# Kernel optimization log

Hardware: AMD Instinct MI355X
Metric: run time of the kernel (lower is better)

## Reference

```python
import jax, jax.numpy as jnp
import numpy as np

N_QUBITS = 6
N_QLAYERS = 3
LOGISTIC_R = 3.99
HENON_A, HENON_B = 1.4, 0.3


def _conv1d(x, w, b):
    # x: [B, C_in, T], w: [C_out, C_in, K=3], SAME padding (pad=1)
    y = jax.lax.conv_general_dilated(x, w, window_strides=(1,), padding=((1, 1),),
                                     dimension_numbers=('NCH', 'OIH', 'NCH'))
    return y + b[None, :, None]


def _apply_1q_batched(state, G, q):
    # state: [B,2,...,2], G: [B,2,2] acting on qubit axis 1+q
    s = jnp.moveaxis(state, 1 + q, -1)
    s = jnp.einsum('bij,b...j->b...i', G, s)
    return jnp.moveaxis(s, -1, 1 + q)


def _apply_1q(state, G, q):
    s = jnp.moveaxis(state, 1 + q, -1)
    s = jnp.einsum('ij,b...j->b...i', G, s)
    return jnp.moveaxis(s, -1, 1 + q)


def _apply_cnot(state, c, t):
    s = jnp.moveaxis(state, (1 + c, 1 + t), (-2, -1))
    # control=1 block: flip target amplitudes
    s = jnp.concatenate([s[..., 0:1, :], s[..., 1:2, ::-1]], axis=-2)
    return jnp.moveaxis(s, (-2, -1), (1 + c, 1 + t))


def quantum_expvals(angles, qweights):
    # angles: [B, 6] real encoding angles; qweights: [3, 6] shared RY params
    B = angles.shape[0]
    state = jnp.zeros((B, 2 ** N_QUBITS), jnp.complex64).at[:, 0].set(1.0)
    state = state.reshape((B,) + (2,) * N_QUBITS)
    half = 0.5 * angles
    for i in range(N_QUBITS):
        ax = half[:, i % N_QUBITS]
        ay = half[:, (i + 1) % N_QUBITS]
        az = half[:, (i + 2) % N_QUBITS]
        cx_, sx_ = jnp.cos(ax), jnp.sin(ax)
        RX = jnp.stack([jnp.stack([cx_ + 0j, -1j * sx_], -1),
                        jnp.stack([-1j * sx_, cx_ + 0j], -1)], -2)
        state = _apply_1q_batched(state, RX, i)
        cy_, sy_ = jnp.cos(ay), jnp.sin(ay)
        RY = jnp.stack([jnp.stack([cy_ + 0j, -sy_ + 0j], -1),
                        jnp.stack([sy_ + 0j, cy_ + 0j], -1)], -2)
        state = _apply_1q_batched(state, RY, i)
        ez = jnp.exp(1j * az)
        zero = jnp.zeros_like(ez)
        RZ = jnp.stack([jnp.stack([jnp.conj(ez), zero], -1),
                        jnp.stack([zero, ez], -1)], -2)
        state = _apply_1q_batched(state, RZ, i)
    for l in range(N_QLAYERS):
        for q in range(N_QUBITS):
            a = 0.5 * qweights[l, q]
            c_, s_ = jnp.cos(a), jnp.sin(a)
            RY = jnp.array([[1., 0.], [0., 1.]], jnp.float32) * c_ + \
                 jnp.array([[0., -1.], [1., 0.]], jnp.float32) * s_
            state = _apply_1q(state, RY.astype(jnp.complex64), q)
        for q in range(N_QUBITS):
            state = _apply_cnot(state, q, (q + 1) % N_QUBITS)
    probs = (state * jnp.conj(state)).real  # [B,2,...,2]
    evs = []
    for i in range(N_QUBITS):
        axes = tuple(a for a in range(1, N_QUBITS + 1) if a != 1 + i)
        p = jnp.sum(probs, axis=axes)  # [B,2]
        evs.append(p[:, 0] - p[:, 1])
    return jnp.stack(evs, -1)  # [B,6]


def _lstm_cell(xt, h, c, Wih, Whh, bih, bhh):
    g = xt @ Wih.T + bih + h @ Whh.T + bhh
    i, f, gg, o = jnp.split(g, 4, axis=-1)
    c2 = jax.nn.sigmoid(f) * c + jax.nn.sigmoid(i) * jnp.tanh(gg)
    h2 = jax.nn.sigmoid(o) * jnp.tanh(c2)
    return h2, c2


def _forward(x, w0, b0, w1, b1, w2, b2, Wih, Whh, bih, bhh, qweights, Wfc, bfc, Wout, bout):
    B = x.shape[0]
    t = x.transpose(0, 2, 1)                 # [B, C, T]
    t = jax.nn.relu(_conv1d(t, w0, b0))
    t = jax.nn.relu(_conv1d(t, w1, b1))
    t = jax.nn.relu(_conv1d(t, w2, b2))
    t = t.transpose(2, 0, 1)                 # [T, B, H]
    H = t.shape[2]
    h0 = jnp.zeros((B, H), x.dtype)
    c0 = jnp.zeros((B, H), x.dtype)

    def step(carry, xt):
        h, c = carry
        h, c = _lstm_cell(xt, h, c, Wih, Whh, bih, bhh)
        h = LOGISTIC_R * h * (1.0 - h)
        x0, y0 = h[:, 0], h[:, 1]
        xn = 1.0 - HENON_A * x0 ** 2 + y0
        yn = HENON_B * x0
        h = jnp.concatenate([xn[:, None], yn[:, None], h[:, 2:]], axis=1)
        # QuantumRNNCell called as qrnn(hx, hx): h = h + fc(quantum(h[:, :6]))
        h = h + quantum_expvals(h[:, :N_QUBITS], qweights) @ Wfc.T + bfc
        return (h, c), None

    (h, _), _ = jax.lax.scan(step, (h0, c0), t)
    return jax.nn.sigmoid(h @ Wout.T + bout)  # [B, 1]


def setup_inputs() -> dict:
    key = jax.random.key(0)
    ks = jax.random.split(key, 20)
    B, T, D, Htcn, Hlstm = 1024, 256, 64, 32, 32
    s = 0.1
    inp = {
        'x': jax.random.normal(ks[0], (B, T, D), jnp.float32),
        'w0': jax.random.normal(ks[1], (Htcn, D, 3), jnp.float32) * s,
        'b0': jax.random.normal(ks[2], (Htcn,), jnp.float32) * s,
        'w1': jax.random.normal(ks[3], (Htcn, Htcn, 3), jnp.float32) * s,
        'b1': jax.random.normal(ks[4], (Htcn,), jnp.float32) * s,
        'w2': jax.random.normal(ks[5], (Htcn, Htcn, 3), jnp.float32) * s,
        'b2': jax.random.normal(ks[6], (Htcn,), jnp.float32) * s,
        'Wih': jax.random.normal(ks[7], (4 * Hlstm, Htcn), jnp.float32) * s,
        'Whh': jax.random.normal(ks[8], (4 * Hlstm, Hlstm), jnp.float32) * s,
        'bih': jax.random.normal(ks[9], (4 * Hlstm,), jnp.float32) * s,
        'bhh': jax.random.normal(ks[10], (4 * Hlstm,), jnp.float32) * s,
        'qweights': jax.random.normal(ks[11], (N_QLAYERS, N_QUBITS), jnp.float32),
        'Wfc': jax.random.normal(ks[12], (Hlstm, N_QUBITS), jnp.float32) * s,
        'bfc': jax.random.normal(ks[13], (Hlstm,), jnp.float32) * s,
        'Wout': jax.random.normal(ks[14], (1, Hlstm), jnp.float32) * s,
        'bout': jax.random.normal(ks[15], (1,), jnp.float32) * s,
    }
    return inp


def reference(x, w0, b0, w1, b1, w2, b2, Wih, Whh, bih, bhh, qweights, Wfc, bfc, Wout, bout):
    return _forward(x, w0, b0, w1, b1, w2, b2, Wih, Whh, bih, bhh, qweights, Wfc, bfc, Wout, bout)
```

## Files before the change

kernel.cpp:

```cpp
#include <hip/hip_runtime.h>

#define B_SIZE 1024
#define T_LEN  256
#define D_IN   64
#define HC     32

typedef int v2i_t __attribute__((ext_vector_type(2)));

__device__ __forceinline__ float frcp(float x){ return __builtin_amdgcn_rcpf(x); }
__device__ __forceinline__ float rfl(float x){
    return __uint_as_float(__builtin_amdgcn_readfirstlane(__float_as_uint(x)));
}
__device__ __forceinline__ float rdlane(float x, int l){
    return __int_as_float(__builtin_amdgcn_readlane(__float_as_int(x), l));
}
__device__ __forceinline__ float ftanh(float x){
    return 1.f - 2.f*frcp(__expf(2.f*x) + 1.f);
}
__device__ __forceinline__ float fsigmoid(float x){
    return frcp(1.f + __expf(-x));
}

template<int CTRL>
__device__ __forceinline__ int dppmov(int x){
    return __builtin_amdgcn_update_dpp(x, x, CTRL, 0xF, 0xF, false);
}

template<int M>
__device__ __forceinline__ int dpp_xor(int x){
    static_assert(M >= 1 && M <= 15, "dpp_xor mask");
    constexpr int hi = M & 12;
    constexpr int q  = (hi == 4 || hi == 12) ? ((M & 3) ^ 3) : (M & 3);
    if constexpr (q == 1) x = dppmov<0xB1>(x);
    else if constexpr (q == 2) x = dppmov<0x4E>(x);
    else if constexpr (q == 3) x = dppmov<0x1B>(x);
    if constexpr (hi == 4)       x = dppmov<0x141>(x);
    else if constexpr (hi == 8)  x = dppmov<0x128>(x);
    else if constexpr (hi == 12) x = dppmov<0x140>(x);
    return x;
}

template<int M>
__device__ __forceinline__ float xshuf(float xf, unsigned lane){
    (void)lane;
    if constexpr (M == 0) return xf;
    int x = __float_as_int(xf);
    if constexpr (M & 16){
        x = __builtin_amdgcn_ds_swizzle(x, ((M & 31) << 10) | 0x1F);
    } else if constexpr (M & 15){
        x = dpp_xor<M & 15>(x);
    }
    if constexpr (M & 32){
        v2i_t r = __builtin_amdgcn_permlane32_swap(x, x, false, false);
        x = r.x ^ r.y ^ x;
    }
    return __int_as_float(x);
}

struct QMasks { int M[3][6]; int S[3][6]; int R[6]; };
constexpr QMasks qmasks(){
    QMasks qm{};
    unsigned m[6], n[6];
    for (int i = 0; i < 6; i++){ m[i] = 1u << i; n[i] = 1u << i; }
    for (int l = 0; l < 3; l++){
        for (int q = 0; q < 6; q++){
            unsigned u = m[q], r = 0;
            for (int i = 0; i < 6; i++) if ((u >> i) & 1u) r |= (32u >> i);
            qm.S[l][q] = (int)r;
            unsigned u2 = 0;
            for (int i = 0; i < 6; i++) u2 |= ((n[i] >> q) & 1u) << i;
            unsigned r2 = 0;
            for (int i = 0; i < 6; i++) if ((u2 >> i) & 1u) r2 |= (32u >> i);
            qm.M[l][q] = (int)r2;
        }
        for (int q = 0; q < 6; q++) m[(q + 1) % 6] ^= m[q];
        n[0] ^= n[5];
        for (int q = 4; q >= 0; q--) n[q + 1] ^= n[q];
    }
    for (int i = 0; i < 6; i++){
        unsigned u = m[i], r = 0;
        for (int j = 0; j < 6; j++) if ((u >> j) & 1u) r |= (32u >> j);
        qm.R[i] = (int)r;
    }
    return qm;
}
constexpr QMasks QM = qmasks();

__global__ __launch_bounds__(256) void conv0_kernel(const float* __restrict__ x,
    const float* __restrict__ w0, const float* __restrict__ b0, float* __restrict__ out)
{
    __shared__ float xs[130*65];
    __shared__ float wl[192*32];
    const int tid = threadIdx.x;
    const int b  = blockIdx.x >> 1;
    const int s0 = (blockIdx.x & 1) * 128;

    for (int idx = tid; idx < 130*64; idx += 256){
        int r = idx >> 6, d = idx & 63;
        int s = s0 - 1 + r;
        float v = 0.f;
        if (s >= 0 && s < T_LEN) v = x[(size_t)b*(T_LEN*D_IN) + (size_t)s*D_IN + d];
        xs[r*65 + d] = v;
    }
    for (int idx = tid; idx < 192*32; idx += 256){
        int r = idx >> 5, c = idx & 31;
        wl[idx] = w0[c*192 + r];
    }
    __syncthreads();

    const int c0 = (tid & 7) * 4;
    const int sl = (tid >> 3) * 4;
    float acc[4][4];
    #pragma unroll
    for (int ci = 0; ci < 4; ci++){
        float bb = b0[c0+ci];
        #pragma unroll
        for (int m = 0; m < 4; m++) acc[ci][m] = bb;
    }
    for (int d = 0; d < 64; d++){
        float xv[6];
        #pragma unroll
        for (int o = 0; o < 6; o++) xv[o] = xs[(sl+o)*65 + d];
        #pragma unroll
        for (int kk = 0; kk < 3; kk++){
            const float4 wv = *(const float4*)&wl[(d*3+kk)*32 + c0];
            float w4[4] = {wv.x, wv.y, wv.z, wv.w};
            #pragma unroll
            for (int ci = 0; ci < 4; ci++)
                #pragma unroll
                for (int m = 0; m < 4; m++)
                    acc[ci][m] += xv[m+kk]*w4[ci];
        }
    }
    #pragma unroll
    for (int ci = 0; ci < 4; ci++){
        float4 v;
        v.x = fmaxf(acc[ci][0], 0.f); v.y = fmaxf(acc[ci][1], 0.f);
        v.z = fmaxf(acc[ci][2], 0.f); v.w = fmaxf(acc[ci][3], 0.f);
        *(float4*)&out[(size_t)b*(HC*T_LEN) + (size_t)(c0+ci)*T_LEN + (s0+sl)] = v;
    }
}

template<bool TOUT>
__global__ __launch_bounds__(256) void convm_kernel(const float* __restrict__ in,
    const float* __restrict__ w, const float* __restrict__ bias, float* __restrict__ out)
{
    __shared__ float xs[130*33];
    __shared__ float wl[96*32];
    const int tid = threadIdx.x;
    const int b  = blockIdx.x >> 1;
    const int s0 = (blockIdx.x & 1) * 128;

    for (int idx = tid; idx < 32*130; idx += 256){
        int ci = idx / 130; int r = idx - ci*130;
        int s = s0 - 1 + r;
        float v = 0.f;
        if (s >= 0 && s < T_LEN) v = in[(size_t)b*(HC*T_LEN) + (size_t)ci*T_LEN + s];
        xs[r*33 + ci] = v;
    }
    for (int idx = tid; idx < 96*32; idx += 256){
        int r = idx >> 5, c = idx & 31;
        wl[idx] = w[c*96 + r];
    }
    __syncthreads();

    const int c0 = (tid & 7) * 4;
    const int sl = (tid >> 3) * 4;
    float acc[4][4];
    #pragma unroll
    for (int ci = 0; ci < 4; ci++){
        float bb = bias[c0+ci];
        #pragma unroll
        for (int m = 0; m < 4; m++) acc[ci][m] = bb;
    }
    for (int ci2 = 0; ci2 < 32; ci2++){
        float xv[6];
        #pragma unroll
        for (int o = 0; o < 6; o++) xv[o] = xs[(sl+o)*33 + ci2];
        #pragma unroll
        for (int kk = 0; kk < 3; kk++){
            const float4 wv = *(const float4*)&wl[(ci2*3+kk)*32 + c0];
            float w4[4] = {wv.x, wv.y, wv.z, wv.w};
            #pragma unroll
            for (int ci = 0; ci < 4; ci++)
                #pragma unroll
                for (int m = 0; m < 4; m++)
                    acc[ci][m] += xv[m+kk]*w4[ci];
        }
    }
    if (!TOUT){
        #pragma unroll
        for (int ci = 0; ci < 4; ci++){
            float4 v;
            v.x = fmaxf(acc[ci][0], 0.f); v.y = fmaxf(acc[ci][1], 0.f);
            v.z = fmaxf(acc[ci][2], 0.f); v.w = fmaxf(acc[ci][3], 0.f);
            *(float4*)&out[(size_t)b*(HC*T_LEN) + (size_t)(c0+ci)*T_LEN + (s0+sl)] = v;
        }
    } else {
        #pragma unroll
        for (int m = 0; m < 4; m++){
            int s = s0 + sl + m;
            float4 v;
            v.x = fmaxf(acc[0][m], 0.f); v.y = fmaxf(acc[1][m], 0.f);
            v.z = fmaxf(acc[2][m], 0.f); v.w = fmaxf(acc[3][m], 0.f);
            *(float4*)&out[(size_t)s*(B_SIZE*HC) + (size_t)b*HC + c0] = v;
        }
    }
}

__global__ __launch_bounds__(256, 1) void scan_kernel(
    const float* __restrict__ tS,
    const float* __restrict__ Wih, const float* __restrict__ Whh,
    const float* __restrict__ bih, const float* __restrict__ bhh,
    const float* __restrict__ qw,  const float* __restrict__ Wfc,
    const float* __restrict__ bfc, const float* __restrict__ Wout,
    const float* __restrict__ bout, float* __restrict__ out)
{
    const unsigned lane = threadIdx.x & 63u;
    const int wv   = threadIdx.x >> 6;
    const int b    = __builtin_amdgcn_readfirstlane(blockIdx.x * 4 + wv);
    const int r1 = lane, r2 = lane + 64;
    const int k  = lane & 31;

    float wA[32], wB[32], uA[32], uB[32];
    #pragma unroll
    for (int j4 = 0; j4 < 8; j4++){
        float4 a  = ((const float4*)Wih)[r1*8 + j4];
        float4 c_ = ((const float4*)Wih)[r2*8 + j4];
        float4 d_ = ((const float4*)Whh)[r1*8 + j4];
        float4 e  = ((const float4*)Whh)[r2*8 + j4];
        wA[j4*4+0]=a.x;  wA[j4*4+1]=a.y;  wA[j4*4+2]=a.z;  wA[j4*4+3]=a.w;
        wB[j4*4+0]=c_.x; wB[j4*4+1]=c_.y; wB[j4*4+2]=c_.z; wB[j4*4+3]=c_.w;
        uA[j4*4+0]=d_.x; uA[j4*4+1]=d_.y; uA[j4*4+2]=d_.z; uA[j4*4+3]=d_.w;
        uB[j4*4+0]=e.x;  uB[j4*4+1]=e.y;  uB[j4*4+2]=e.z;  uB[j4*4+3]=e.w;
    }
    const float bias1 = bih[r1] + bhh[r1];
    const float bias2 = bih[r2] + bhh[r2];

    float wfcr[6];
    #pragma unroll
    for (int j = 0; j < 6; j++) wfcr[j] = Wfc[k*6 + j];
    const float bfcl  = bfc[k];
    const float woutl = (lane < 32) ? Wout[k] : 0.f;
    const float boutv = bout[0];

    float cgv[18], ssin[18];
    #pragma unroll
    for (int g = 0; g < 18; g++){
        int l = g / 6, q = g % 6;
        float a = 0.5f * qw[g];
        float cv = __cosf(a), sv = __sinf(a);
        cgv[g] = rfl(cv);
        unsigned sm = (unsigned)QM.S[l][q];
        ssin[g] = (__builtin_popcount(sm & lane) & 1) ? sv : -sv;
    }
    float wsgn[6];
    #pragma unroll
    for (int j = 0; j < 6; j++) wsgn[j] = (lane & (1u << j)) ? -1.f : 1.f;
    const bool qs[6] = { (lane & 32u) != 0, (lane & 16u) != 0, (lane & 8u) != 0,
                         (lane & 4u) != 0,  (lane & 2u) != 0,  (lane & 1u) != 0 };

    float h = 0.f, c = 0.f;
    const float* xbase = tS + (size_t)b * HC;

    float4 xf[8];
    #pragma unroll
    for (int j4 = 0; j4 < 8; j4++) xf[j4] = ((const float4*)xbase)[j4];

    #pragma clang loop unroll(disable)
    for (int s = 0; s < T_LEN; s++){
        float xt[32];
        #pragma unroll
        for (int j4 = 0; j4 < 8; j4++){
            xt[j4*4+0]=xf[j4].x; xt[j4*4+1]=xf[j4].y; xt[j4*4+2]=xf[j4].z; xt[j4*4+3]=xf[j4].w;
        }
        {
            int s2 = (s + 1 < T_LEN) ? s + 1 : s;
            const float4* np_ = (const float4*)(xbase + (size_t)s2*(B_SIZE*HC));
            #pragma unroll
            for (int j4 = 0; j4 < 8; j4++) xf[j4] = np_[j4];
        }

        float a1a = bias1, a1b = 0.f, a2a = bias2, a2b = 0.f;
        #pragma unroll
        for (int j = 0; j < 32; j += 2){
            a1a += xt[j]*wA[j];     a1b += xt[j+1]*wA[j+1];
            a2a += xt[j]*wB[j];     a2b += xt[j+1]*wB[j+1];
        }
        #pragma unroll
        for (int j = 0; j < 32; j += 2){
            float h0 = rdlane(h, j), h1 = rdlane(h, j+1);
            a1a += h0*uA[j];   a1b += h1*uA[j+1];
            a2a += h0*uB[j];   a2b += h1*uB[j+1];
        }
        float acc1 = a1a + a1b, acc2 = a2a + a2b;

        float sigA = fsigmoid(acc1);
        float argB = (lane < 32) ? acc2 : 0.5f*acc2;
        float tt   = ftanh(argB);
        float actB = (lane < 32) ? tt : (0.5f + 0.5f*tt);
        float fsig = xshuf<32>(sigA, lane);
        float osig = xshuf<32>(actB, lane);
        c = fsig*c + sigA*actB;
        float hn = osig * ftanh(c);

        hn = 3.99f * hn * (1.f - hn);
        float x0 = rdlane(hn, 0), y0 = rdlane(hn, 1);
        float xnv = 1.f - 1.4f*x0*x0 + y0;
        float ynv = 0.3f * x0;

        float ang[6];
        ang[0] = 0.5f*xnv; ang[1] = 0.5f*ynv;
        ang[2] = 0.5f*rdlane(hn, 2); ang[3] = 0.5f*rdlane(hn, 3);
        ang[4] = 0.5f*rdlane(hn, 4); ang[5] = 0.5f*rdlane(hn, 5);
        float ca[6], sa[6];
        #pragma unroll
        for (int j = 0; j < 6; j++){ ca[j] = __cosf(ang[j]); sa[j] = __sinf(ang[j]); }

        float fr[6], fi[6];
        #pragma unroll
        for (int i = 0; i < 6; i++){
            const int i1 = (i+1)%6, i2 = (i+2)%6;
            float cx=ca[i], sx=sa[i], cy=ca[i1], sy=sa[i1], cz=ca[i2], sz=sa[i2];
            float w0r = cy*cx, w0i = sy*sx;
            float w1r = sy*cx, w1i = -cy*sx;
            float q0r = cz*w0r + sz*w0i, q0i = cz*w0i - sz*w0r;
            float q1r = cz*w1r - sz*w1i, q1i = cz*w1i + sz*w1r;
            fr[i] = qs[i] ? q1r : q0r;
            fi[i] = qs[i] ? q1i : q0i;
        }
        float t01r = fr[0]*fr[1] - fi[0]*fi[1], t01i = fr[0]*fi[1] + fi[0]*fr[1];
        float t23r = fr[2]*fr[3] - fi[2]*fi[3], t23i = fr[2]*fi[3] + fi[2]*fr[3];
        float t45r = fr[4]*fr[5] - fi[4]*fi[5], t45i = fr[4]*fi[5] + fi[4]*fr[5];
        float t03r = t01r*t23r - t01i*t23i,     t03i = t01r*t23i + t01i*t23r;
        float ar   = t03r*t45r - t03i*t45i,     ai   = t03r*t45i + t03i*t45r;

        #define GATE(L,Q) { \
            constexpr int MM = QM.M[L][Q]; \
            float br = xshuf<MM>(ar, lane), bi = xshuf<MM>(ai, lane); \
            float cg = cgv[(L)*6+(Q)], ss = ssin[(L)*6+(Q)]; \
            ar = cg*ar + ss*br; ai = cg*ai + ss*bi; }
        GATE(0,0) GATE(0,1) GATE(0,2) GATE(0,3) GATE(0,4) GATE(0,5)
        GATE(1,0) GATE(1,1) GATE(1,2) GATE(1,3) GATE(1,4) GATE(1,5)
        GATE(2,0) GATE(2,1) GATE(2,2) GATE(2,3) GATE(2,4) GATE(2,5)
        #undef GATE

        float wp = ar*ar + ai*ai;
        wp = wsgn[0]*wp + xshuf< 1>(wp, lane);
        wp = wsgn[1]*wp + xshuf< 2>(wp, lane);
        wp = wsgn[2]*wp + xshuf< 4>(wp, lane);
        wp = wsgn[3]*wp + xshuf< 8>(wp, lane);
        wp = wsgn[4]*wp + xshuf<16>(wp, lane);
        wp = wsgn[5]*wp + xshuf<32>(wp, lane);
        float ev0 = rdlane(wp, QM.R[0]), ev1 = rdlane(wp, QM.R[1]);
        float ev2 = rdlane(wp, QM.R[2]), ev3 = rdlane(wp, QM.R[3]);
        float ev4 = rdlane(wp, QM.R[4]), ev5 = rdlane(wp, QM.R[5]);

        float upd = bfcl + (wfcr[0]*ev0 + wfcr[1]*ev1)
                         + (wfcr[2]*ev2 + wfcr[3]*ev3)
                         + (wfcr[4]*ev4 + wfcr[5]*ev5);

        float hsel = hn;
        hsel = (lane == 0u) ? xnv : hsel;
        hsel = (lane == 1u) ? ynv : hsel;
        h = hsel + upd;
    }

    float pv = (lane < 32) ? h*woutl : 0.f;
    #pragma unroll
    for (int off = 32; off; off >>= 1) pv += __shfl_xor(pv, off, 64);
    if (lane == 0) out[b] = fsigmoid(pv + boutv);
}

extern "C" void kernel_launch(void* const* d_in, const int* in_sizes, int n_in,
                              void* d_out, int out_size, void* d_ws, size_t ws_size,
                              hipStream_t stream)
{
    (void)in_sizes; (void)n_in; (void)out_size; (void)ws_size;
    const float* x    = (const float*)d_in[0];
    const float* w0   = (const float*)d_in[1];
    const float* b0   = (const float*)d_in[2];
    const float* w1   = (const float*)d_in[3];
    const float* b1   = (const float*)d_in[4];
    const float* w2   = (const float*)d_in[5];
    const float* b2   = (const float*)d_in[6];
    const float* Wih  = (const float*)d_in[7];
    const float* Whh  = (const float*)d_in[8];
    const float* bih  = (const float*)d_in[9];
    const float* bhh  = (const float*)d_in[10];
    const float* qw   = (const float*)d_in[11];
    const float* Wfc  = (const float*)d_in[12];
    const float* bfc  = (const float*)d_in[13];
    const float* Wout = (const float*)d_in[14];
    const float* bout = (const float*)d_in[15];
    float* out = (float*)d_out;

    float* t0 = (float*)d_ws;
    float* t1 = t0 + (size_t)B_SIZE*HC*T_LEN;
    float* tS = t0;

    conv0_kernel<<<2048, 256, 0, stream>>>(x, w0, b0, t0);
    convm_kernel<false><<<2048, 256, 0, stream>>>(t0, w1, b1, t1);
    convm_kernel<true ><<<2048, 256, 0, stream>>>(t1, w2, b2, tS);
    scan_kernel<<<256, 256, 0, stream>>>(tS, Wih, Whh, bih, bhh, qw, Wfc, bfc, Wout, bout, out);
}
```

Before: 681.0 us.

## Hoist LSTM input projection out of recurrent scan into parallel gates kernel

```diff
diff --git a/kernel.cpp b/kernel.cpp
--- a/kernel.cpp
+++ b/kernel.cpp
@@ -5,7 +5,8 @@
 #define D_IN   64
 #define HC     32
 
-typedef int v2i_t __attribute__((ext_vector_type(2)));
+typedef int   v2i_t __attribute__((ext_vector_type(2)));
+typedef float v2f   __attribute__((ext_vector_type(2)));
 
 __device__ __forceinline__ float frcp(float x){ return __builtin_amdgcn_rcpf(x); }
 __device__ __forceinline__ float rfl(float x){
@@ -40,15 +41,24 @@
     return x;
 }
 
+#if defined(__has_builtin)
+#  if __has_builtin(__builtin_amdgcn_permlane16_swap)
+#    define HAVE_PL16 1
+#  endif
+#endif
+
 template<int M>
-__device__ __forceinline__ float xshuf(float xf, unsigned lane){
-    (void)lane;
+__device__ __forceinline__ float xshuf(float xf){
     if constexpr (M == 0) return xf;
     int x = __float_as_int(xf);
+    if constexpr (M & 15) x = dpp_xor<M & 15>(x);
     if constexpr (M & 16){
-        x = __builtin_amdgcn_ds_swizzle(x, ((M & 31) << 10) | 0x1F);
-    } else if constexpr (M & 15){
-        x = dpp_xor<M & 15>(x);
+#ifdef HAVE_PL16
+        v2i_t r = __builtin_amdgcn_permlane16_swap(x, x, false, false);
+        x = r.x ^ r.y ^ x;
+#else
+        x = __builtin_amdgcn_ds_swizzle(x, (16 << 10) | 0x1F);
+#endif
     }
     if constexpr (M & 32){
         v2i_t r = __builtin_amdgcn_permlane32_swap(x, x, false, false);
@@ -208,7 +218,183 @@
     }
 }
 
+__global__ __launch_bounds__(256) void gates_kernel(const float* __restrict__ tS,
+    const float* __restrict__ Wih, const float* __restrict__ bih,
+    const float* __restrict__ bhh, float* __restrict__ G)
+{
+    __shared__ float xs[8][32];
+    const int tid = threadIdx.x;
+    const size_t pair0 = (size_t)blockIdx.x * 8;
+
+    { int p = tid >> 5, j = tid & 31;
+      xs[p][j] = tS[pair0*32 + (size_t)p*32 + j]; }
+    __syncthreads();
+
+    const int r = tid & 127;
+    const int half = tid >> 7;
+    float4 wr[8];
+    #pragma unroll
+    for (int j4 = 0; j4 < 8; j4++) wr[j4] = ((const float4*)Wih)[r*8 + j4];
+    const float br = bih[r] + bhh[r];
+
+    #pragma unroll
+    for (int pp = 0; pp < 4; pp++){
+        const int p = half + pp*2;
+        float a0 = br, a1 = 0.f, a2 = 0.f, a3 = 0.f;
+        #pragma unroll
+        for (int j4 = 0; j4 < 8; j4++){
+            const float4 xv = *(const float4*)&xs[p][j4*4];
+            a0 += wr[j4].x*xv.x; a1 += wr[j4].y*xv.y;
+            a2 += wr[j4].z*xv.z; a3 += wr[j4].w*xv.w;
+        }
+        G[(pair0 + p)*128 + r] = (a0+a1)+(a2+a3);
+    }
+}
+
 __global__ __launch_bounds__(256, 1) void scan_kernel(
+    const float* __restrict__ G,   const float* __restrict__ Whh,
+    const float* __restrict__ qw,  const float* __restrict__ Wfc,
+    const float* __restrict__ bfc, const float* __restrict__ Wout,
+    const float* __restrict__ bout, float* __restrict__ out)
+{
+    const unsigned lane = threadIdx.x & 63u;
+    const int wv   = threadIdx.x >> 6;
+    const int b    = __builtin_amdgcn_readfirstlane(blockIdx.x * 4 + wv);
+    const int r1 = lane, r2 = lane + 64;
+    const int k  = lane & 31;
+
+    v2f uAB[32];
+    #pragma unroll
+    for (int j4 = 0; j4 < 8; j4++){
+        float4 d_ = ((const float4*)Whh)[r1*8 + j4];
+        float4 e  = ((const float4*)Whh)[r2*8 + j4];
+        uAB[j4*4+0] = v2f{d_.x, e.x}; uAB[j4*4+1] = v2f{d_.y, e.y};
+        uAB[j4*4+2] = v2f{d_.z, e.z}; uAB[j4*4+3] = v2f{d_.w, e.w};
+    }
+
+    float wfcr[6];
+    #pragma unroll
+    for (int j = 0; j < 6; j++) wfcr[j] = Wfc[k*6 + j];
+    const float bfcl  = bfc[k];
+    const float woutl = (lane < 32) ? Wout[k] : 0.f;
+    const float boutv = bout[0];
+
+    float cgv[18], ssin[18];
+    #pragma unroll
+    for (int g = 0; g < 18; g++){
+        int l = g / 6, q = g % 6;
+        float a = 0.5f * qw[g];
+        float cv = __cosf(a), sv = __sinf(a);
+        cgv[g] = rfl(cv);
+        unsigned sm = (unsigned)QM.S[l][q];
+        ssin[g] = (__builtin_popcount(sm & lane) & 1) ? sv : -sv;
+    }
+    float wsgn[6];
+    #pragma unroll
+    for (int j = 0; j < 6; j++) wsgn[j] = (lane & (1u << j)) ? -1.f : 1.f;
+    const bool qs[6] = { (lane & 32u) != 0, (lane & 16u) != 0, (lane & 8u) != 0,
+                         (lane & 4u) != 0,  (lane & 2u) != 0,  (lane & 1u) != 0 };
+
+    float h = 0.f, c = 0.f;
+    const float* gbase = G + (size_t)b*128;
+    float g1 = gbase[r1], g2 = gbase[r2];
+
+    #pragma clang loop unroll(disable)
+    for (int s = 0; s < T_LEN; s++){
+        const float cg1 = g1, cg2 = g2;
+        {
+            int s2 = (s + 1 < T_LEN) ? s + 1 : s;
+            const float* gn = gbase + (size_t)s2*(B_SIZE*128);
+            g1 = gn[r1]; g2 = gn[r2];
+        }
+
+        v2f a0 = v2f{cg1, cg2}, a1 = v2f{0.f,0.f}, a2 = v2f{0.f,0.f}, a3 = v2f{0.f,0.f};
+        #pragma unroll
+        for (int j = 0; j < 32; j += 4){
+            float h0 = rdlane(h, j),   h1 = rdlane(h, j+1);
+            float h2 = rdlane(h, j+2), h3 = rdlane(h, j+3);
+            a0 += h0*uAB[j]; a1 += h1*uAB[j+1]; a2 += h2*uAB[j+2]; a3 += h3*uAB[j+3];
+        }
+        v2f accv = (a0+a1)+(a2+a3);
+        float acc1 = accv.x, acc2 = accv.y;
+
+        float sigA = fsigmoid(acc1);
+        float argB = (lane < 32) ? acc2 : 0.5f*acc2;
+        float tt   = ftanh(argB);
+        float actB = (lane < 32) ? tt : (0.5f + 0.5f*tt);
+        float fsig = xshuf<32>(sigA);
+        float osig = xshuf<32>(actB);
+        c = fsig*c + sigA*actB;
+        float hn = osig * ftanh(c);
+
+        hn = 3.99f * hn * (1.f - hn);
+        float x0 = rdlane(hn, 0), y0 = rdlane(hn, 1);
+        float xnv = 1.f - 1.4f*x0*x0 + y0;
+        float ynv = 0.3f * x0;
+
+        float ang[6];
+        ang[0] = 0.5f*xnv; ang[1] = 0.5f*ynv;
+        ang[2] = 0.5f*rdlane(hn, 2); ang[3] = 0.5f*rdlane(hn, 3);
+        ang[4] = 0.5f*rdlane(hn, 4); ang[5] = 0.5f*rdlane(hn, 5);
+        float ca[6], sa[6];
+        #pragma unroll
+        for (int j = 0; j < 6; j++){ ca[j] = __cosf(ang[j]); sa[j] = __sinf(ang[j]); }
+
+        float fr[6], fi[6];
+        #pragma unroll
+        for (int i = 0; i < 6; i++){
+            const int i1 = (i+1)%6, i2 = (i+2)%6;
+            float cx=ca[i], sx=sa[i], cy=ca[i1], sy=sa[i1], cz=ca[i2], sz=sa[i2];
+            float w0r = cy*cx, w0i = sy*sx;
+            float w1r = sy*cx, w1i = -cy*sx;
+            float q0r = cz*w0r + sz*w0i, q0i = cz*w0i - sz*w0r;
+            float q1r = cz*w1r - sz*w1i, q1i = cz*w1i + sz*w1r;
+            fr[i] = qs[i] ? q1r : q0r;
+            fi[i] = qs[i] ? q1i : q0i;
+        }
+        v2f t01 = v2f{fr[0]*fr[1] - fi[0]*fi[1], fr[0]*fi[1] + fi[0]*fr[1]};
+        v2f t23 = v2f{fr[2]*fr[3] - fi[2]*fi[3], fr[2]*fi[3] + fi[2]*fr[3]};
+        v2f t45 = v2f{fr[4]*fr[5] - fi[4]*fi[5], fr[4]*fi[5] + fi[4]*fr[5]};
+        v2f t03 = v2f{t01.x*t23.x - t01.y*t23.y, t01.x*t23.y + t01.y*t23.x};
+        v2f av  = v2f{t03.x*t45.x - t03.y*t45.y, t03.x*t45.y + t03.y*t45.x};
+
+        #define GATE(L,Q) { \
+            constexpr int MM = QM.M[L][Q]; \
+            v2f bv; bv.x = xshuf<MM>(av.x); bv.y = xshuf<MM>(av.y); \
+            av = cgv[(L)*6+(Q)]*av + ssin[(L)*6+(Q)]*bv; }
+        GATE(0,0) GATE(0,1) GATE(0,2) GATE(0,3) GATE(0,4) GATE(0,5)
+        GATE(1,0) GATE(1,1) GATE(1,2) GATE(1,3) GATE(1,4) GATE(1,5)
+        GATE(2,0) GATE(2,1) GATE(2,2) GATE(2,3) GATE(2,4) GATE(2,5)
+        #undef GATE
+
+        float wp = av.x*av.x + av.y*av.y;
+        wp = wsgn[0]*wp + xshuf< 1>(wp);
+        wp = wsgn[1]*wp + xshuf< 2>(wp);
+        wp = wsgn[2]*wp + xshuf< 4>(wp);
+        wp = wsgn[3]*wp + xshuf< 8>(wp);
+        wp = wsgn[4]*wp + xshuf<16>(wp);
+        wp = wsgn[5]*wp + xshuf<32>(wp);
+        float ev0 = rdlane(wp, QM.R[0]), ev1 = rdlane(wp, QM.R[1]);
+        float ev2 = rdlane(wp, QM.R[2]), ev3 = rdlane(wp, QM.R[3]);
+        float ev4 = rdlane(wp, QM.R[4]), ev5 = rdlane(wp, QM.R[5]);
+
+        float upd = bfcl + (wfcr[0]*ev0 + wfcr[1]*ev1)
+                         + (wfcr[2]*ev2 + wfcr[3]*ev3)
+                         + (wfcr[4]*ev4 + wfcr[5]*ev5);
+
+        float hsel = hn;
+        hsel = (lane == 0u) ? xnv : hsel;
+        hsel = (lane == 1u) ? ynv : hsel;
+        h = hsel + upd;
+    }
+
+    float pv = (lane < 32) ? h*woutl : 0.f;
+    #pragma unroll
+    for (int off = 32; off; off >>= 1) pv += __shfl_xor(pv, off, 64);
+    if (lane == 0) out[b] = fsigmoid(pv + boutv);
+}
+
+__global__ __launch_bounds__(256, 1) void scan_legacy(
     const float* __restrict__ tS,
     const float* __restrict__ Wih, const float* __restrict__ Whh,
     const float* __restrict__ bih, const float* __restrict__ bhh,
@@ -299,8 +485,8 @@
         float argB = (lane < 32) ? acc2 : 0.5f*acc2;
         float tt   = ftanh(argB);
         float actB = (lane < 32) ? tt : (0.5f + 0.5f*tt);
-        float fsig = xshuf<32>(sigA, lane);
-        float osig = xshuf<32>(actB, lane);
+        float fsig = xshuf<32>(sigA);
+        float osig = xshuf<32>(actB);
         c = fsig*c + sigA*actB;
         float hn = osig * ftanh(c);
 
@@ -337,7 +523,7 @@
 
         #define GATE(L,Q) { \
             constexpr int MM = QM.M[L][Q]; \
-            float br = xshuf<MM>(ar, lane), bi = xshuf<MM>(ai, lane); \
+            float br = xshuf<MM>(ar), bi = xshuf<MM>(ai); \
             float cg = cgv[(L)*6+(Q)], ss = ssin[(L)*6+(Q)]; \
             ar = cg*ar + ss*br; ai = cg*ai + ss*bi; }
         GATE(0,0) GATE(0,1) GATE(0,2) GATE(0,3) GATE(0,4) GATE(0,5)
@@ -346,12 +532,12 @@
         #undef GATE
 
         float wp = ar*ar + ai*ai;
-        wp = wsgn[0]*wp + xshuf< 1>(wp, lane);
-        wp = wsgn[1]*wp + xshuf< 2>(wp, lane);
-        wp = wsgn[2]*wp + xshuf< 4>(wp, lane);
-        wp = wsgn[3]*wp + xshuf< 8>(wp, lane);
-        wp = wsgn[4]*wp + xshuf<16>(wp, lane);
-        wp = wsgn[5]*wp + xshuf<32>(wp, lane);
+        wp = wsgn[0]*wp + xshuf< 1>(wp);
+        wp = wsgn[1]*wp + xshuf< 2>(wp);
+        wp = wsgn[2]*wp + xshuf< 4>(wp);
+        wp = wsgn[3]*wp + xshuf< 8>(wp);
+        wp = wsgn[4]*wp + xshuf<16>(wp);
+        wp = wsgn[5]*wp + xshuf<32>(wp);
         float ev0 = rdlane(wp, QM.R[0]), ev1 = rdlane(wp, QM.R[1]);
         float ev2 = rdlane(wp, QM.R[2]), ev3 = rdlane(wp, QM.R[3]);
         float ev4 = rdlane(wp, QM.R[4]), ev5 = rdlane(wp, QM.R[5]);
@@ -376,7 +562,7 @@
                               void* d_out, int out_size, void* d_ws, size_t ws_size,
                               hipStream_t stream)
 {
-    (void)in_sizes; (void)n_in; (void)out_size; (void)ws_size;
+    (void)in_sizes; (void)n_in; (void)out_size;
     const float* x    = (const float*)d_in[0];
     const float* w0   = (const float*)d_in[1];
     const float* b0   = (const float*)d_in[2];
@@ -395,12 +581,20 @@
     const float* bout = (const float*)d_in[15];
     float* out = (float*)d_out;
 
+    const size_t tensorN = (size_t)B_SIZE*HC*T_LEN;
     float* t0 = (float*)d_ws;
-    float* t1 = t0 + (size_t)B_SIZE*HC*T_LEN;
+    float* t1 = t0 + tensorN;
     float* tS = t0;
+    float* G  = t1 + tensorN;
+    const size_t need = (2*tensorN + (size_t)T_LEN*B_SIZE*128) * sizeof(float);
 
     conv0_kernel<<<2048, 256, 0, stream>>>(x, w0, b0, t0);
     convm_kernel<false><<<2048, 256, 0, stream>>>(t0, w1, b1, t1);
     convm_kernel<true ><<<2048, 256, 0, stream>>>(t1, w2, b2, tS);
-    scan_kernel<<<256, 256, 0, stream>>>(tS, Wih, Whh, bih, bhh, qw, Wfc, bfc, Wout, bout, out);
-}
+    if (ws_size >= need){
+        gates_kernel<<<(T_LEN*B_SIZE)/8, 256, 0, stream>>>(tS, Wih, bih, bhh, G);
+        scan_kernel<<<256, 256, 0, stream>>>(G, Whh, qw, Wfc, bfc, Wout, bout, out);
+    } else {
+        scan_legacy<<<256, 256, 0, stream>>>(tS, Wih, Whh, bih, bhh, qw, Wfc, bfc, Wout, bout, out);
+    }
+}
```

New measurement: 747.6 us. 9.8% more time.
